# Performance work log

Hardware: AMD Instinct MI355X
Metric: run time of the kernel (lower is better)

The kernel has to match this reference:

```python
import jax, jax.numpy as jnp
from jax import lax
import numpy as np

HID = 128      # hidden_dim / mamba d_model
DI = 256       # d_inner = expand*HID
DS = 16        # d_state
DTR = 8        # dt_rank = ceil(HID/16)
DEPTH = 3
DCONV = 4


def conv2d(x, w, b):
    # x [B,C,H,W], w [O,I,3,3], SAME padding, stride 1
    y = lax.conv_general_dilated(x, w, (1, 1), 'SAME',
                                 dimension_numbers=('NCHW', 'OIHW', 'NCHW'))
    return y + b[None, :, None, None]


def gelu(x):
    return jax.nn.gelu(x, approximate=False)


def mamba_layer(x, in_w, conv_w, conv_b, xproj_w, dt_w, dt_b, Alog, Dp, out_w):
    # x: [B, L, HID]  (Mamba S6 block, no internal residual)
    B, L, _ = x.shape
    xz = x @ in_w.T                      # [B,L,2*DI]
    xs, z = jnp.split(xz, 2, axis=-1)    # [B,L,DI] each
    # depthwise causal conv1d, kernel DCONV, left-pad DCONV-1
    xpad = jnp.pad(xs, ((0, 0), (DCONV - 1, 0), (0, 0)))
    xc = lax.conv_general_dilated(xpad.transpose(0, 2, 1), conv_w[:, None, :],
                                  (1,), 'VALID', feature_group_count=DI,
                                  dimension_numbers=('NCH', 'OIH', 'NCH'))
    u = jax.nn.silu((xc + conv_b[None, :, None]).transpose(0, 2, 1))  # [B,L,DI]
    proj = u @ xproj_w.T                                              # [B,L,DTR+2*DS]
    dt, Bm, Cm = jnp.split(proj, [DTR, DTR + DS], axis=-1)
    delta = jax.nn.softplus(dt @ dt_w.T + dt_b)                       # [B,L,DI]
    A = -jnp.exp(Alog)                                                # [DI,DS]

    def step(h, inp):
        d_t, B_t, C_t, u_t = inp                 # [B,DI],[B,DS],[B,DS],[B,DI]
        dA = jnp.exp(d_t[..., None] * A)         # [B,DI,DS]
        h = dA * h + (d_t * u_t)[..., None] * B_t[:, None, :]
        y = jnp.einsum('bds,bs->bd', h, C_t)
        return h, y

    h0 = jnp.zeros((B, DI, DS), x.dtype)
    xs_seq = (delta.transpose(1, 0, 2), Bm.transpose(1, 0, 2),
              Cm.transpose(1, 0, 2), u.transpose(1, 0, 2))
    _, ys = lax.scan(step, h0, xs_seq)           # ys [L,B,DI]
    y = ys.transpose(1, 0, 2) + u * Dp           # D skip connection
    y = y * jax.nn.silu(z)
    return y @ out_w.T                           # [B,L,HID]


def forward(x, enc1_w, enc1_b, enc2_w, enc2_b,
            m_in_w, m_conv_w, m_conv_b, m_xproj_w, m_dt_w, m_dt_b,
            m_Alog, m_D, m_out_w, fus_w, fus_b,
            pred1_w, pred1_b, pred2_w, pred2_b):
    b, c, h, w = x.shape
    feats = conv2d(gelu(conv2d(x, enc1_w, enc1_b)), enc2_w, enc2_b)  # [b,HID,h,w]

    # scan along h: 'b c h w -> (b w) h c'
    sh = feats.transpose(0, 3, 2, 1).reshape(b * w, h, HID)
    for i in range(DEPTH):
        sh = mamba_layer(sh, m_in_w[i], m_conv_w[i], m_conv_b[i], m_xproj_w[i],
                         m_dt_w[i], m_dt_b[i], m_Alog[i], m_D[i], m_out_w[i])
    feats_h = sh.reshape(b, w, h, HID).transpose(0, 3, 2, 1)

    # scan along w: 'b c h w -> (b h) w c' (same shared mamba layers)
    sw = feats.transpose(0, 2, 3, 1).reshape(b * h, w, HID)
    for i in range(DEPTH):
        sw = mamba_layer(sw, m_in_w[i], m_conv_w[i], m_conv_b[i], m_xproj_w[i],
                         m_dt_w[i], m_dt_b[i], m_Alog[i], m_D[i], m_out_w[i])
    feats_w = sw.reshape(b, h, w, HID).transpose(0, 3, 1, 2)

    fused = conv2d(feats_h + feats_w, fus_w, fus_b)
    pred = conv2d(gelu(conv2d(fused, pred1_w, pred1_b)), pred2_w, pred2_b)
    return pred  # [b, spectral_bands, h, w]


def setup_inputs():
    key = jax.random.key(0)
    ks = jax.random.split(key, 16)
    s = 0.05

    def n(k, shape):
        return jax.random.normal(k, shape, jnp.float32) * s

    inp = {}
    inp['x'] = jax.random.normal(ks[0], (1, 1, 128, 128), jnp.float32)
    inp['enc1_w'] = n(ks[1], (HID, 1, 3, 3)); inp['enc1_b'] = jnp.zeros((HID,), jnp.float32)
    inp['enc2_w'] = n(ks[2], (HID, HID, 3, 3)); inp['enc2_b'] = jnp.zeros((HID,), jnp.float32)
    inp['m_in_w'] = n(ks[3], (DEPTH, 2 * DI, HID))
    inp['m_conv_w'] = n(ks[4], (DEPTH, DI, DCONV))
    inp['m_conv_b'] = jnp.zeros((DEPTH, DI), jnp.float32)
    inp['m_xproj_w'] = n(ks[5], (DEPTH, DTR + 2 * DS, DI))
    inp['m_dt_w'] = n(ks[6], (DEPTH, DI, DTR))
    inp['m_dt_b'] = jnp.full((DEPTH, DI), -3.0, jnp.float32)
    Alog = jnp.log(jnp.tile(jnp.arange(1, DS + 1, dtype=jnp.float32), (DI, 1)))
    inp['m_Alog'] = jnp.broadcast_to(Alog, (DEPTH, DI, DS)).copy()
    inp['m_D'] = jnp.ones((DEPTH, DI), jnp.float32)
    inp['m_out_w'] = n(ks[7], (DEPTH, HID, DI))
    inp['fus_w'] = n(ks[8], (HID, HID, 3, 3)); inp['fus_b'] = jnp.zeros((HID,), jnp.float32)
    inp['pred1_w'] = n(ks[9], (HID, HID, 3, 3)); inp['pred1_b'] = jnp.zeros((HID,), jnp.float32)
    inp['pred2_w'] = n(ks[10], (1, HID, 3, 3)); inp['pred2_b'] = jnp.zeros((1,), jnp.float32)
    return inp


def reference(x, enc1_w, enc1_b, enc2_w, enc2_b,
              m_in_w, m_conv_w, m_conv_b, m_xproj_w, m_dt_w, m_dt_b,
              m_Alog, m_D, m_out_w, fus_w, fus_b,
              pred1_w, pred1_b, pred2_w, pred2_b):
    return forward(x, enc1_w, enc1_b, enc2_w, enc2_b,
                   m_in_w, m_conv_w, m_conv_b, m_xproj_w, m_dt_w, m_dt_b,
                   m_Alog, m_D, m_out_w, fus_w, fus_b,
                   pred1_w, pred1_b, pred2_w, pred2_b)
```

## Files before the change

kernel.cpp:

```cpp
#include <hip/hip_runtime.h>
#include <math.h>

#define NTOK 16384

typedef __attribute__((ext_vector_type(8))) short bf16x8;
typedef __attribute__((ext_vector_type(4))) float f32x4;

__device__ __forceinline__ float geluf(float x){
    return 0.5f*x*(1.0f+erff(x*0.70710678118654752f));
}
__device__ __forceinline__ float siluf(float x){
    return x/(1.0f+__expf(-x));
}
__device__ __forceinline__ float softplusf(float x){
    return (x>20.0f)? x : log1pf(__expf(x));
}
__device__ __forceinline__ void split_bf16(float x, unsigned short& h, unsigned short& l){
    union { float f; unsigned u; } c; c.f = x;
    h = (unsigned short)(c.u >> 16);
    union { unsigned u; float f; } hf; hf.u = c.u & 0xffff0000u;
    union { float f; unsigned u; } rc; rc.f = x - hf.f;
    l = (unsigned short)(rc.u >> 16);
}

template<bool GELU_OUT>
__global__ __launch_bounds__(256) void conv3x3_kernel(
    const float* __restrict__ in, const float* __restrict__ wgt,
    const float* __restrict__ bias, float* __restrict__ out,
    int CI, int CO)
{
    __shared__ float tile[18][68];
    const int tx = threadIdx.x & 15;
    const int ty = threadIdx.x >> 4;
    const int w0 = blockIdx.x * 64;
    const int h0 = blockIdx.y * 16;
    const int cog = blockIdx.z * 8;

    float acc[8][4];
    #pragma unroll
    for (int i=0;i<8;i++){
        float b = (cog+i < CO) ? bias[cog+i] : 0.f;
        #pragma unroll
        for (int j=0;j<4;j++) acc[i][j] = b;
    }

    for (int ci=0; ci<CI; ci++){
        const float* inp = in + ci*16384;
        for (int e = threadIdx.x; e < 18*66; e += 256){
            int r = e/66, cc = e - r*66;
            int hh = h0 - 1 + r, ww = w0 - 1 + cc;
            float v = 0.f;
            if ((unsigned)hh < 128u && (unsigned)ww < 128u) v = inp[hh*128+ww];
            tile[r][cc] = v;
        }
        __syncthreads();
        float rin[3][8];
        #pragma unroll
        for (int r=0;r<3;r++){
            float4 a = *(const float4*)&tile[ty+r][tx*4];
            float4 b = *(const float4*)&tile[ty+r][tx*4+4];
            rin[r][0]=a.x; rin[r][1]=a.y; rin[r][2]=a.z; rin[r][3]=a.w;
            rin[r][4]=b.x; rin[r][5]=b.y; rin[r][6]=b.z; rin[r][7]=b.w;
        }
        #pragma unroll
        for (int co=0; co<8; co++){
            if (cog+co < CO) {
                const float* wp = wgt + ((cog+co)*CI + ci)*9;
                #pragma unroll
                for (int r=0;r<3;r++){
                    #pragma unroll
                    for (int dx=0;dx<3;dx++){
                        float wv = wp[r*3+dx];
                        #pragma unroll
                        for (int j=0;j<4;j++)
                            acc[co][j] = fmaf(wv, rin[r][j+dx], acc[co][j]);
                    }
                }
            }
        }
        __syncthreads();
    }
    const int h = h0 + ty;
    const int wbase = w0 + tx*4;
    #pragma unroll
    for (int co=0; co<8; co++){
        if (cog+co < CO){
            float t0 = acc[co][0], t1 = acc[co][1], t2 = acc[co][2], t3 = acc[co][3];
            if (GELU_OUT){ t0=geluf(t0); t1=geluf(t1); t2=geluf(t2); t3=geluf(t3); }
            *(float4*)&out[(cog+co)*16384 + h*128 + wbase] = make_float4(t0,t1,t2,t3);
        }
    }
}

__global__ __launch_bounds__(256) void wsplit_kernel(
    const float* __restrict__ wgt, unsigned short* __restrict__ whi,
    unsigned short* __restrict__ wlo)
{
    int e = blockIdx.x*256 + threadIdx.x;
    int ci = e & 127, co = (e >> 7) & 127, t = e >> 14;
    float v = wgt[((co<<7)|ci)*9 + t];
    unsigned short h, l; split_bf16(v, h, l);
    int cog = co >> 4, lr = co & 15;
    int chk = ci >> 5, kg = (ci >> 3) & 3, j = ci & 7;
    int o = ((((t*8 + cog)*4 + chk)*4 + kg)*16 + lr)*8 + j;
    whi[o] = h; wlo[o] = l;
}

template<bool GELU_OUT>
__global__ __launch_bounds__(256) void conv_mfma_kernel(
    const float* __restrict__ in, const unsigned short* __restrict__ whi,
    const unsigned short* __restrict__ wlo, const float* __restrict__ bias,
    float* __restrict__ out)
{
    __shared__ unsigned short sHi[6*20*40], sLo[6*20*40];
    const int tid  = threadIdx.x;
    const int wave = tid >> 6;
    const int lane = tid & 63;
    const int wr   = wave >> 1;
    const int wc   = wave & 1;
    const int lr   = lane & 15;
    const int kg   = lane >> 4;
    const int w0   = blockIdx.x * 16;
    const int h0   = blockIdx.y * 4;
    const int cogz = blockIdx.z * 4;

    f32x4 acc[2][2];
    #pragma unroll
    for (int cg=0;cg<2;cg++)
        #pragma unroll
        for (int pg=0;pg<2;pg++)
            acc[cg][pg] = (f32x4){0.f,0.f,0.f,0.f};

    for (int ch = 0; ch < 4; ch++){
        const int cc0 = ch*32;
        for (int e = tid; e < 3456; e += 256){
            int cil = e / 108;
            int rem = e - cil*108;
            int hl  = rem / 18;
            int wl  = rem - hl*18;
            int hh = h0 - 1 + hl, ww = w0 - 1 + wl;
            float v = 0.f;
            if ((unsigned)hh < 128u && (unsigned)ww < 128u)
                v = in[(size_t)(cc0+cil)*16384 + hh*128 + ww];
            unsigned short hi, lo; split_bf16(v, hi, lo);
            int o = (hl*20 + wl)*40 + cil;
            sHi[o] = hi; sLo[o] = lo;
        }
        __syncthreads();
        #pragma unroll
        for (int dy=0; dy<3; dy++){
            #pragma unroll
            for (int dx=0; dx<3; dx++){
                const int t = dy*3+dx;
                bf16x8 ah[2], al[2], bh[2], bl[2];
                #pragma unroll
                for (int cg=0; cg<2; cg++){
                    int cog = cogz + wr*2 + cg;
                    size_t off = ((size_t)(((t*8 + cog)*4 + ch)*4 + kg)*16 + lr)*8;
                    ah[cg] = *(const bf16x8*)&whi[off];
                    al[cg] = *(const bf16x8*)&wlo[off];
                }
                #pragma unroll
                for (int pg=0; pg<2; pg++){
                    int g = wc*2 + pg;
                    int o = ((g+dy)*20 + lr + dx)*40 + kg*8;
                    bh[pg] = *(const bf16x8*)&sHi[o];
                    bl[pg] = *(const bf16x8*)&sLo[o];
                }
                #pragma unroll
                for (int cg=0; cg<2; cg++){
                    #pragma unroll
                    for (int pg=0; pg<2; pg++){
                        acc[cg][pg] = __builtin_amdgcn_mfma_f32_16x16x32_bf16(ah[cg], bh[pg], acc[cg][pg], 0,0,0);
                        acc[cg][pg] = __builtin_amdgcn_mfma_f32_16x16x32_bf16(ah[cg], bl[pg], acc[cg][pg], 0,0,0);
                        acc[cg][pg] = __builtin_amdgcn_mfma_f32_16x16x32_bf16(al[cg], bh[pg], acc[cg][pg], 0,0,0);
                    }
                }
            }
        }
        __syncthreads();
    }
    #pragma unroll
    for (int cg=0; cg<2; cg++){
        #pragma unroll
        for (int pg=0; pg<2; pg++){
            int h = h0 + wc*2 + pg;
            int w = w0 + lr;
            #pragma unroll
            for (int r=0; r<4; r++){
                int co = (cogz + wr*2 + cg)*16 + kg*4 + r;
                float v = acc[cg][pg][r] + bias[co];
                if (GELU_OUT) v = geluf(v);
                out[(size_t)co*16384 + h*128 + w] = v;
            }
        }
    }
}

__global__ __launch_bounds__(256) void conv3x3_co1_kernel(
    const float* __restrict__ in, const float* __restrict__ wgt,
    const float* __restrict__ bias, float* __restrict__ out, int CI)
{
    __shared__ float tile[16][4][128];
    const int h0 = blockIdx.x*2;
    const int hl = threadIdx.x >> 7;
    const int w  = threadIdx.x & 127;
    float acc = bias[0];
    for (int cc0 = 0; cc0 < CI; cc0 += 16){
        for (int e = threadIdx.x; e < 2048; e += 256){
            int c4 = e & 31, r = (e>>5)&3, ci = e>>7;
            int hh = h0 - 1 + r;
            float4 v = make_float4(0.f,0.f,0.f,0.f);
            if ((unsigned)hh < 128u)
                v = *(const float4*)&in[(size_t)(cc0+ci)*16384 + hh*128 + c4*4];
            *(float4*)&tile[ci][r][c4*4] = v;
        }
        __syncthreads();
        #pragma unroll 4
        for (int ci=0; ci<16; ci++){
            float w_s[9];
            #pragma unroll
            for (int k=0;k<9;k++) w_s[k] = wgt[(size_t)(cc0+ci)*9 + k];
            #pragma unroll
            for (int r=0;r<3;r++){
                #pragma unroll
                for (int dx=0;dx<3;dx++){
                    int col = w + dx - 1;
                    float x = ((unsigned)col < 128u) ? tile[ci][hl+r][col] : 0.f;
                    acc = fmaf(w_s[r*3+dx], x, acc);
                }
            }
        }
        __syncthreads();
    }
    out[(size_t)(h0+hl)*128 + w] = acc;
}

__global__ __launch_bounds__(256) void gemm_mfma_kernel(
    const float* __restrict__ A, const float* __restrict__ W,
    float* __restrict__ C, int M, int N, int K, int lda)
{
    __shared__ unsigned short Ah[64*48], Al[64*48], Bh[64*48], Bl[64*48];
    const int tid  = threadIdx.x;
    const int wave = tid >> 6;
    const int lane = tid & 63;
    const int wr   = wave >> 1;
    const int wc   = wave & 1;
    const int lrow = lane & 15;
    const int kg   = lane >> 4;

    const int m0 = blockIdx.x * 64;
    const int n0 = blockIdx.y * 64;

    f32x4 acc[2][2];
    #pragma unroll
    for (int mi=0;mi<2;mi++)
        #pragma unroll
        for (int ni=0;ni<2;ni++)
            acc[mi][ni] = (f32x4){0.f,0.f,0.f,0.f};

    for (int k0 = 0; k0 < K; k0 += 32){
        #pragma unroll
        for (int it=0; it<2; it++){
            int idx = tid + it*256;
            int r = idx >> 3, c4 = idx & 7;
            float4 v = *(const float4*)&A[(size_t)(m0+r)*lda + k0 + c4*4];
            unsigned short h[4], l[4];
            split_bf16(v.x, h[0], l[0]);
            split_bf16(v.y, h[1], l[1]);
            split_bf16(v.z, h[2], l[2]);
            split_bf16(v.w, h[3], l[3]);
            *(uint2*)&Ah[r*48 + c4*4] = make_uint2(h[0]|((unsigned)h[1]<<16), h[2]|((unsigned)h[3]<<16));
            *(uint2*)&Al[r*48 + c4*4] = make_uint2(l[0]|((unsigned)l[1]<<16), l[2]|((unsigned)l[3]<<16));
        }
        #pragma unroll
        for (int it=0; it<2; it++){
            int idx = tid + it*256;
            int r = idx >> 3, c4 = idx & 7;
            float4 v = make_float4(0.f,0.f,0.f,0.f);
            if (n0 + r < N) v = *(const float4*)&W[(size_t)(n0+r)*K + k0 + c4*4];
            unsigned short h[4], l[4];
            split_bf16(v.x, h[0], l[0]);
            split_bf16(v.y, h[1], l[1]);
            split_bf16(v.z, h[2], l[2]);
            split_bf16(v.w, h[3], l[3]);
            *(uint2*)&Bh[r*48 + c4*4] = make_uint2(h[0]|((unsigned)h[1]<<16), h[2]|((unsigned)h[3]<<16));
            *(uint2*)&Bl[r*48 + c4*4] = make_uint2(l[0]|((unsigned)l[1]<<16), l[2]|((unsigned)l[3]<<16));
        }
        __syncthreads();

        bf16x8 fah[2], fal[2], fbh[2], fbl[2];
        #pragma unroll
        for (int mi=0;mi<2;mi++){
            int row = (wr*2+mi)*16 + lrow;
            fah[mi] = *(const bf16x8*)&Ah[row*48 + kg*8];
            fal[mi] = *(const bf16x8*)&Al[row*48 + kg*8];
        }
        #pragma unroll
        for (int ni=0;ni<2;ni++){
            int row = (wc*2+ni)*16 + lrow;
            fbh[ni] = *(const bf16x8*)&Bh[row*48 + kg*8];
            fbl[ni] = *(const bf16x8*)&Bl[row*48 + kg*8];
        }
        #pragma unroll
        for (int mi=0;mi<2;mi++){
            #pragma unroll
            for (int ni=0;ni<2;ni++){
                acc[mi][ni] = __builtin_amdgcn_mfma_f32_16x16x32_bf16(fah[mi], fbh[ni], acc[mi][ni], 0,0,0);
                acc[mi][ni] = __builtin_amdgcn_mfma_f32_16x16x32_bf16(fah[mi], fbl[ni], acc[mi][ni], 0,0,0);
                acc[mi][ni] = __builtin_amdgcn_mfma_f32_16x16x32_bf16(fal[mi], fbh[ni], acc[mi][ni], 0,0,0);
            }
        }
        __syncthreads();
    }
    #pragma unroll
    for (int mi=0;mi<2;mi++){
        #pragma unroll
        for (int ni=0;ni<2;ni++){
            int n = n0 + (wc*2+ni)*16 + lrow;
            if (n < N){
                #pragma unroll
                for (int r=0;r<4;r++){
                    int m = m0 + (wr*2+mi)*16 + kg*4 + r;
                    C[(size_t)m*N + n] = acc[mi][ni][r];
                }
            }
        }
    }
}

__global__ __launch_bounds__(256) void conv1d_silu_kernel(
    const float* __restrict__ xz, const float* __restrict__ cw,
    const float* __restrict__ cb, float* __restrict__ U)
{
    const int m = blockIdx.x;
    const int d = threadIdx.x;
    const int t = m & 127;
    float4 w4 = *(const float4*)&cw[d*4];
    float wj[4] = {w4.x, w4.y, w4.z, w4.w};
    float s = cb[d];
    #pragma unroll
    for (int j=0;j<4;j++){
        int tt = t - 3 + j;
        if (tt >= 0) s = fmaf(wj[j], xz[(size_t)(m - 3 + j)*512 + d], s);
    }
    U[(size_t)m*256 + d] = siluf(s);
}

__global__ __launch_bounds__(64) void scan_fused_kernel(
    const float* __restrict__ usrc, const float* __restrict__ zsrc,
    float* __restrict__ ydst, const float* __restrict__ proj,
    const float* __restrict__ dtw, const float* __restrict__ dtb,
    const float* __restrict__ Alog, const float* __restrict__ Dp)
{
    __shared__ float sP[128*40];
    const int b = blockIdx.y;
    const int d = blockIdx.x*64 + threadIdx.x;

    {
        const float4* src = (const float4*)(proj + (size_t)b*128*40);
        float4* dst = (float4*)sP;
        #pragma unroll
        for (int i=0;i<20;i++)
            dst[threadIdx.x + i*64] = src[threadIdx.x + i*64];
    }

    float A[16], h[16];
    #pragma unroll
    for (int s=0;s<16;s++){ A[s] = -__expf(Alog[d*16+s]); h[s]=0.f; }
    float4 dw0 = *(const float4*)&dtw[d*8];
    float4 dw1 = *(const float4*)&dtw[d*8+4];
    const float dtbv = dtb[d];
    const float Dv = Dp[d];
    const int m0 = b*128;

    float uvp[8], zvp[8];
    #pragma unroll
    for (int k=0;k<8;k++){
        int m = m0 + k;
        uvp[k] = usrc[(size_t)m*256 + d];
        zvp[k] = zsrc[(size_t)m*512 + d];
    }
    __syncthreads();

    for (int t0=0; t0<128; t0+=8){
        #pragma unroll
        for (int k=0;k<8;k++){
            const int t = t0 + k;
            const int m = m0 + t;
            float uv = uvp[k], zv = zvp[k];
            const int mf = m0 + ((t+8 < 128) ? (t+8) : 127);
            uvp[k] = usrc[(size_t)mf*256 + d];
            zvp[k] = zsrc[(size_t)mf*512 + d];

            const float* p = &sP[t*40];
            float4 P0 = *(const float4*)(p);
            float4 P1 = *(const float4*)(p+4);
            float dta = fmaf(P0.x,dw0.x, fmaf(P0.y,dw0.y, dtbv));
            float dtb2= fmaf(P0.z,dw0.z, P0.w*dw0.w);
            float dtc = fmaf(P1.x,dw1.x, P1.y*dw1.y);
            float dtd = fmaf(P1.z,dw1.z, P1.w*dw1.w);
            float dv = softplusf((dta+dtb2)+(dtc+dtd));
            float du = dv*uv;
            float4 B0 = *(const float4*)(p+8),  B1 = *(const float4*)(p+12),
                   B2 = *(const float4*)(p+16), B3 = *(const float4*)(p+20);
            float4 C0 = *(const float4*)(p+24), C1 = *(const float4*)(p+28),
                   C2 = *(const float4*)(p+32), C3 = *(const float4*)(p+36);
            const float Bv[16] = {B0.x,B0.y,B0.z,B0.w, B1.x,B1.y,B1.z,B1.w,
                                  B2.x,B2.y,B2.z,B2.w, B3.x,B3.y,B3.z,B3.w};
            const float Cv[16] = {C0.x,C0.y,C0.z,C0.w, C1.x,C1.y,C1.z,C1.w,
                                  C2.x,C2.y,C2.z,C2.w, C3.x,C3.y,C3.z,C3.w};
            float yp[4] = {0.f,0.f,0.f,0.f};
            #pragma unroll
            for (int s=0;s<16;s++){
                float dA = __expf(dv*A[s]);
                h[s] = fmaf(dA, h[s], du*Bv[s]);
                yp[s&3] = fmaf(h[s], Cv[s], yp[s&3]);
            }
            float y = (yp[0]+yp[1])+(yp[2]+yp[3]);
            ydst[(size_t)m*512 + d] = (y + uv*Dv) * siluf(zv);
        }
    }
}

__global__ __launch_bounds__(256) void transpose_cw_kernel(
    const float* __restrict__ feats, float* __restrict__ out,
    int ows, int ohs)
{
    __shared__ float tile[32][33];
    const int h = blockIdx.z;
    const int c0 = blockIdx.y*32, w0 = blockIdx.x*32;
    const int lx = threadIdx.x & 31, ly = threadIdx.x >> 5;
    #pragma unroll
    for (int i=0;i<4;i++){
        int c = c0 + ly + i*8;
        tile[ly+i*8][lx] = feats[(size_t)c*16384 + h*128 + w0 + lx];
    }
    __syncthreads();
    #pragma unroll
    for (int i=0;i<4;i++){
        int w = w0 + ly + i*8;
        out[(size_t)w*ows + (size_t)h*ohs + c0 + lx] = tile[lx][ly+i*8];
    }
}

__global__ __launch_bounds__(256) void fuse_transpose_kernel(
    const float* __restrict__ XH, const float* __restrict__ XW,
    float* __restrict__ FH)
{
    __shared__ float tile[32][33];
    const int h = blockIdx.z;
    const int c0 = blockIdx.y*32, w0 = blockIdx.x*32;
    const int lx = threadIdx.x & 31, ly = threadIdx.x >> 5;
    #pragma unroll
    for (int i=0;i<4;i++){
        int w = w0 + ly + i*8;
        float v = XH[(size_t)w*16384 + h*128 + c0 + lx]
                + XW[(size_t)h*16384 + w*128 + c0 + lx];
        tile[ly+i*8][lx] = v;
    }
    __syncthreads();
    #pragma unroll
    for (int i=0;i<4;i++){
        int c = c0 + ly + i*8;
        FH[(size_t)c*16384 + h*128 + w0 + lx] = tile[lx][ly+i*8];
    }
}

extern "C" void kernel_launch(void* const* d_in, const int* in_sizes, int n_in,
                              void* d_out, int out_size, void* d_ws, size_t ws_size,
                              hipStream_t stream)
{
    const float* x        = (const float*)d_in[0];
    const float* enc1_w   = (const float*)d_in[1];
    const float* enc1_b   = (const float*)d_in[2];
    const float* enc2_w   = (const float*)d_in[3];
    const float* enc2_b   = (const float*)d_in[4];
    const float* m_in_w   = (const float*)d_in[5];
    const float* m_conv_w = (const float*)d_in[6];
    const float* m_conv_b = (const float*)d_in[7];
    const float* m_xproj_w= (const float*)d_in[8];
    const float* m_dt_w   = (const float*)d_in[9];
    const float* m_dt_b   = (const float*)d_in[10];
    const float* m_Alog   = (const float*)d_in[11];
    const float* m_D      = (const float*)d_in[12];
    const float* m_out_w  = (const float*)d_in[13];
    const float* fus_w    = (const float*)d_in[14];
    const float* fus_b    = (const float*)d_in[15];
    const float* pred1_w  = (const float*)d_in[16];
    const float* pred1_b  = (const float*)d_in[17];
    const float* pred2_w  = (const float*)d_in[18];
    const float* pred2_b  = (const float*)d_in[19];
    float* out = (float*)d_out;

    float* ws    = (float*)d_ws;
    float* FEATS = ws;
    float* XH    = ws +  2u*1024*1024;
    float* XW    = ws +  4u*1024*1024;
    float* XZ    = ws +  6u*1024*1024;
    float* U     = ws + 14u*1024*1024;
    float* PROJ  = ws + 18u*1024*1024;
    float* T0 = XZ;
    float* FH = XZ;
    float* G1 = XZ + 2u*1024*1024;
    float* G2 = XZ + 4u*1024*1024;
    unsigned short* EHI = (unsigned short*)(ws + 10u*1024*1024);
    unsigned short* ELO = EHI + 147456;
    unsigned short* FHI = (unsigned short*)(ws + 12u*1024*1024);
    unsigned short* FLO = FHI + 147456;
    unsigned short* PHI = FLO + 147456;
    unsigned short* PLO = PHI + 147456;

    const dim3 cmgrid(8, 32, 2);

    conv3x3_kernel<true ><<<dim3(2,8,16), 256, 0, stream>>>(x, enc1_w, enc1_b, T0, 1, 128);
    wsplit_kernel<<<576, 256, 0, stream>>>(enc2_w, EHI, ELO);
    conv_mfma_kernel<false><<<cmgrid, 256, 0, stream>>>(T0, EHI, ELO, enc2_b, FEATS);

    transpose_cw_kernel<<<dim3(4,4,128), 256, 0, stream>>>(FEATS, XH, 16384, 128);
    transpose_cw_kernel<<<dim3(4,4,128), 256, 0, stream>>>(FEATS, XW, 128, 16384);

    for (int pass = 0; pass < 2; pass++){
        float* Xact = pass ? XW : XH;
        for (int l = 0; l < 3; l++){
            gemm_mfma_kernel<<<dim3(256,8), 256, 0, stream>>>(Xact, m_in_w + (size_t)l*512*128, XZ, NTOK, 512, 128, 128);
            conv1d_silu_kernel<<<NTOK, 256, 0, stream>>>(XZ, m_conv_w + (size_t)l*256*4, m_conv_b + (size_t)l*256, U);
            gemm_mfma_kernel<<<dim3(256,1), 256, 0, stream>>>(U, m_xproj_w + (size_t)l*40*256, PROJ, NTOK, 40, 256, 256);
            scan_fused_kernel<<<dim3(4,128), 64, 0, stream>>>(U, XZ + 256, XZ, PROJ,
                m_dt_w + (size_t)l*256*8, m_dt_b + (size_t)l*256,
                m_Alog + (size_t)l*256*16, m_D + (size_t)l*256);
            gemm_mfma_kernel<<<dim3(256,2), 256, 0, stream>>>(XZ, m_out_w + (size_t)l*128*256, Xact, NTOK, 128, 256, 512);
        }
    }

    fuse_transpose_kernel<<<dim3(4,4,128), 256, 0, stream>>>(XH, XW, FH);

    wsplit_kernel<<<576, 256, 0, stream>>>(fus_w, FHI, FLO);
    conv_mfma_kernel<false><<<cmgrid, 256, 0, stream>>>(FH, FHI, FLO, fus_b, G1);
    wsplit_kernel<<<576, 256, 0, stream>>>(pred1_w, PHI, PLO);
    conv_mfma_kernel<true ><<<cmgrid, 256, 0, stream>>>(G1, PHI, PLO, pred1_b, G2);
    conv3x3_co1_kernel<<<64, 256, 0, stream>>>(G2, pred2_w, pred2_b, out, 128);
}
```

Measured before the change: 1.178 ms.

## Split selective-scan state dimension across four lanes with shuffle reduction

The selective-scan kernel now assigns four threads per channel, each owning four of the sixteen state entries, and combines the partial outputs with two xor-shuffles. The grid grows from 512 to 2048 wavefronts, which exposes more parallelism for the serial recurrence and cuts per-thread register state. In exchange, the dt projection, softplus and u/z loads are computed redundantly in each of the four lanes, and only one lane in four writes the output.

```diff
diff --git a/kernel.cpp b/kernel.cpp
--- a/kernel.cpp
+++ b/kernel.cpp
@@ -347,15 +347,17 @@
     U[(size_t)m*256 + d] = siluf(s);
 }
 
-__global__ __launch_bounds__(64) void scan_fused_kernel(
+__global__ __launch_bounds__(64) void scan_s4_kernel(
     const float* __restrict__ usrc, const float* __restrict__ zsrc,
     float* __restrict__ ydst, const float* __restrict__ proj,
     const float* __restrict__ dtw, const float* __restrict__ dtb,
     const float* __restrict__ Alog, const float* __restrict__ Dp)
 {
     __shared__ float sP[128*40];
-    const int b = blockIdx.y;
-    const int d = blockIdx.x*64 + threadIdx.x;
+    const int b  = blockIdx.y;
+    const int dl = threadIdx.x >> 2;
+    const int sg = threadIdx.x & 3;
+    const int d  = blockIdx.x*16 + dl;
 
     {
         const float4* src = (const float4*)(proj + (size_t)b*128*40);
@@ -365,31 +367,31 @@
             dst[threadIdx.x + i*64] = src[threadIdx.x + i*64];
     }
 
-    float A[16], h[16];
-    #pragma unroll
-    for (int s=0;s<16;s++){ A[s] = -__expf(Alog[d*16+s]); h[s]=0.f; }
+    float A[4], h[4];
+    #pragma unroll
+    for (int j=0;j<4;j++){ A[j] = -__expf(Alog[d*16 + sg*4 + j]); h[j]=0.f; }
     float4 dw0 = *(const float4*)&dtw[d*8];
     float4 dw1 = *(const float4*)&dtw[d*8+4];
     const float dtbv = dtb[d];
     const float Dv = Dp[d];
     const int m0 = b*128;
 
-    float uvp[8], zvp[8];
-    #pragma unroll
-    for (int k=0;k<8;k++){
+    float uvp[4], zvp[4];
+    #pragma unroll
+    for (int k=0;k<4;k++){
         int m = m0 + k;
         uvp[k] = usrc[(size_t)m*256 + d];
         zvp[k] = zsrc[(size_t)m*512 + d];
     }
     __syncthreads();
 
-    for (int t0=0; t0<128; t0+=8){
-        #pragma unroll
-        for (int k=0;k<8;k++){
+    for (int t0=0; t0<128; t0+=4){
+        #pragma unroll
+        for (int k=0;k<4;k++){
             const int t = t0 + k;
             const int m = m0 + t;
             float uv = uvp[k], zv = zvp[k];
-            const int mf = m0 + ((t+8 < 128) ? (t+8) : 127);
+            const int mf = m0 + ((t+4 < 128) ? (t+4) : 127);
             uvp[k] = usrc[(size_t)mf*256 + d];
             zvp[k] = zsrc[(size_t)mf*512 + d];
 
@@ -402,23 +404,21 @@
             float dtd = fmaf(P1.z,dw1.z, P1.w*dw1.w);
             float dv = softplusf((dta+dtb2)+(dtc+dtd));
             float du = dv*uv;
-            float4 B0 = *(const float4*)(p+8),  B1 = *(const float4*)(p+12),
-                   B2 = *(const float4*)(p+16), B3 = *(const float4*)(p+20);
-            float4 C0 = *(const float4*)(p+24), C1 = *(const float4*)(p+28),
-                   C2 = *(const float4*)(p+32), C3 = *(const float4*)(p+36);
-            const float Bv[16] = {B0.x,B0.y,B0.z,B0.w, B1.x,B1.y,B1.z,B1.w,
-                                  B2.x,B2.y,B2.z,B2.w, B3.x,B3.y,B3.z,B3.w};
-            const float Cv[16] = {C0.x,C0.y,C0.z,C0.w, C1.x,C1.y,C1.z,C1.w,
-                                  C2.x,C2.y,C2.z,C2.w, C3.x,C3.y,C3.z,C3.w};
-            float yp[4] = {0.f,0.f,0.f,0.f};
+            float4 Bq = *(const float4*)(p + 8 + sg*4);
+            float4 Cq = *(const float4*)(p + 24 + sg*4);
+            float Bv[4] = {Bq.x,Bq.y,Bq.z,Bq.w};
+            float Cv[4] = {Cq.x,Cq.y,Cq.z,Cq.w};
+            float y = 0.f;
             #pragma unroll
-            for (int s=0;s<16;s++){
-                float dA = __expf(dv*A[s]);
-                h[s] = fmaf(dA, h[s], du*Bv[s]);
-                yp[s&3] = fmaf(h[s], Cv[s], yp[s&3]);
-            }
-            float y = (yp[0]+yp[1])+(yp[2]+yp[3]);
-            ydst[(size_t)m*512 + d] = (y + uv*Dv) * siluf(zv);
+            for (int j=0;j<4;j++){
+                float dA = __expf(dv*A[j]);
+                h[j] = fmaf(dA, h[j], du*Bv[j]);
+                y = fmaf(h[j], Cv[j], y);
+            }
+            y += __shfl_xor(y, 1);
+            y += __shfl_xor(y, 2);
+            if (sg == 0)
+                ydst[(size_t)m*512 + d] = (y + uv*Dv) * siluf(zv);
         }
     }
 }
@@ -526,7 +526,7 @@
             gemm_mfma_kernel<<<dim3(256,8), 256, 0, stream>>>(Xact, m_in_w + (size_t)l*512*128, XZ, NTOK, 512, 128, 128);
             conv1d_silu_kernel<<<NTOK, 256, 0, stream>>>(XZ, m_conv_w + (size_t)l*256*4, m_conv_b + (size_t)l*256, U);
             gemm_mfma_kernel<<<dim3(256,1), 256, 0, stream>>>(U, m_xproj_w + (size_t)l*40*256, PROJ, NTOK, 40, 256, 256);
-            scan_fused_kernel<<<dim3(4,128), 64, 0, stream>>>(U, XZ + 256, XZ, PROJ,
+            scan_s4_kernel<<<dim3(16,128), 64, 0, stream>>>(U, XZ + 256, XZ, PROJ,
                 m_dt_w + (size_t)l*256*8, m_dt_b + (size_t)l*256,
                 m_Alog + (size_t)l*256*16, m_D + (size_t)l*256);
             gemm_mfma_kernel<<<dim3(256,2), 256, 0, stream>>>(XZ, m_out_w + (size_t)l*128*256, Xact, NTOK, 128, 256, 512);
```

After: 1.271 ms. 1.08x slower.
